# Kernel tuning notes

Hardware: AMD Instinct MI355X
Metric: run time of the kernel (lower is better)

The kernel has to match this reference:

```python
import jax, jax.numpy as jnp
import numpy as np

B, L, F, H, NC = 128, 1024, 128, 64, 16


def setup_inputs() -> dict:
    key = jax.random.key(0)
    ks = jax.random.split(key, 8)
    # strictly increasing timestamps -> each unique_consecutive group holds exactly
    # one event, so the torch group-mean over agg_c_t is a plain per-event update.
    t = jnp.broadcast_to(jnp.arange(L, dtype=jnp.float32), (B, L))
    m = jax.random.randint(ks[0], (B, L), 0, F).astype(jnp.float32)  # feature ids stored as float
    x = jax.random.normal(ks[1], (B, L), dtype=jnp.float32)
    delt = jax.random.uniform(ks[2], (B, L), dtype=jnp.float32)
    X = jnp.stack([t, m, x, delt], axis=1)  # [B, 4, L]
    lengths = jnp.full((B,), L, dtype=jnp.int32)
    s = 1.0 / np.sqrt(H + 1)
    W_gates = jax.random.uniform(ks[3], (F, 4 * H, H + 1), minval=-s, maxval=s)  # per-feature Linear(H+1 -> 4H)
    b_gates = jax.random.uniform(ks[4], (F, 4 * H), minval=-s, maxval=s)
    w_decay = jax.random.uniform(ks[5], (F,), minval=-1.0, maxval=1.0)  # per-feature Linear(1 -> 1)
    b_decay = jax.random.uniform(ks[6], (F,), minval=-1.0, maxval=1.0)
    in_dim = F * H + H  # concat(c_t, h_t.flatten()) -- default output branch
    so = 1.0 / np.sqrt(in_dim)
    W_out = jax.random.uniform(ks[7], (NC, in_dim), minval=-so, maxval=so)
    b_out = jnp.zeros((NC,), dtype=jnp.float32)
    return dict(X=X, lengths=lengths, W_gates=W_gates, b_gates=b_gates,
                w_decay=w_decay, b_decay=b_decay, W_out=W_out, b_out=b_out)


def _run_sample(x, delt, m, length, W_gates, b_gates, w_decay, b_decay):
    """Event-wise recurrence for one sample; returns concat(c_t, h_t.flatten())."""
    L_ = x.shape[0]
    F_, _, Hp1 = W_gates.shape
    H_ = Hp1 - 1

    def step(carry, ev):
        h_t, c_t = carry                     # h_t: [F,H], c_t: [H]
        mj, xj, dj, valid = ev
        # gated per-feature decay: exp(-max(0, w*dt + b)) (sr == 1)
        decay = jnp.exp(-jnp.maximum(0.0, w_decay[mj] * dj + b_decay[mj]))
        h_dec = decay * h_t[mj]
        inp = jnp.concatenate([xj[None], h_dec])            # [H+1]
        gates = W_gates[mj] @ inp + b_gates[mj]             # [4H]
        gi, gf, go, gc = jnp.split(gates, 4)
        c_new = jax.nn.sigmoid(gf) * c_t + jax.nn.sigmoid(gi) * jnp.tanh(gc)
        h_row = jax.nn.sigmoid(go) * jnp.tanh(c_new)
        c_t = jnp.where(valid, c_new, c_t)
        h_t = h_t.at[mj].set(jnp.where(valid, h_row, h_t[mj]))
        return (h_t, c_t), None

    valid = jnp.arange(L_) < length
    init = (jnp.zeros((F_, H_), x.dtype), jnp.zeros((H_,), x.dtype))
    (h_t, c_t), _ = jax.lax.scan(step, init, (m, x, delt, valid))
    return jnp.concatenate([c_t, h_t.reshape(-1)])          # [F*H + H]


def reference(X, lengths, W_gates, b_gates, w_decay, b_decay, W_out, b_out):
    m = X[:, 1].astype(jnp.int32)
    x = X[:, 2]
    delt = X[:, 3]
    feat = jax.vmap(lambda xi, di, mi, li: _run_sample(
        xi, di, mi, li, W_gates, b_gates, w_decay, b_decay))(x, delt, m, lengths)
    logits = feat @ W_out.T + b_out                          # [B, n_class]
    return jax.nn.softmax(logits, axis=-1)                   # torch softmax(dim=0) on 1-D vec per sample
```

## Files before the change

### kernel.cpp

```cpp
#include <hip/hip_runtime.h>
#include <cstdint>
#include <cstddef>

#define Bn 128
#define Ln 1024
#define Fn 128
#define Hn 64
#define NGn 256
#define NCn 16
#define IN_DIM (Hn + Fn*Hn)
#define NT 512
#define NREF 7

typedef float    f32x4 __attribute__((ext_vector_type(4)));
typedef float    f32x2 __attribute__((ext_vector_type(2)));
typedef _Float16 f16x8 __attribute__((ext_vector_type(8)));
typedef _Float16 f16x2 __attribute__((ext_vector_type(2)));

union U8 { f16x8 v; f16x2 p[4]; };

#define OFF_G    0
#define OFF_H    131072
#define OFF_PK   147456
#define OFF_MF   155648
#define OFF_PV   156672
#define OFF_NX   158720
#define OFF_RDY  160768
#define OFF_DON  161792
#define OFF_C    162816
#define OFF_RED  163072
#define OFF_LOG  163584
#define LDS_TOTAL 163648

__device__ __forceinline__ float fsigm(float x) {
    return __fdividef(1.0f, 1.0f + __expf(-x));
}
__device__ __forceinline__ float ftanh(float x) {
    float e = __expf(2.0f * x);
    return 1.0f - __fdividef(2.0f, e + 1.0f);
}
__device__ __forceinline__ float sigm_slow(float x) { return 1.0f / (1.0f + expf(-x)); }

#if __has_builtin(__builtin_amdgcn_fdot2)
#define DOT2(WP, HP, ACC) __builtin_amdgcn_fdot2((WP), (HP), (ACC), false)
#else
#define DOT2(WP, HP, ACC) fmaf((float)(WP)[0], (float)(HP)[0], \
                               fmaf((float)(WP)[1], (float)(HP)[1], (ACC)))
#endif

__global__ __launch_bounds__(256)
void prep_f16(const float* __restrict__ Wg, const float* __restrict__ bg,
              f16x8* __restrict__ Gw, f32x2* __restrict__ Gwb)
{
    const int m = blockIdx.x, r = threadIdx.x;
    const float* src = Wg + ((size_t)m * NGn + r) * 65;
    f32x2 wb; wb[0] = src[0]; wb[1] = bg[m * NGn + r];
    Gwb[((size_t)m << 8) + r] = wb;
#pragma unroll
    for (int c = 0; c < 8; ++c) {
        f16x8 v;
#pragma unroll
        for (int e = 0; e < 8; ++e) v[e] = (_Float16)src[1 + 8 * c + e];
        Gw[((size_t)m << 11) + (c << 8) + r] = v;
    }
}

__global__ __launch_bounds__(NT, 1)
void lstm_pre(const float* __restrict__ X, const int* __restrict__ lengths,
              const f16x8* __restrict__ Gw, const f32x2* __restrict__ Gwb,
              const float* __restrict__ wdec, const float* __restrict__ bdec,
              const float* __restrict__ Wo, const float* __restrict__ bo,
              float* __restrict__ out)
{
    extern __shared__ char smem[];
    float*    G_s  = (float*)(smem + OFF_G);
    _Float16* h16  = (_Float16*)(smem + OFF_H);
    f32x2*    pk_s = (f32x2*)(smem + OFF_PK);
    unsigned char* mf_s = (unsigned char*)(smem + OFF_MF);
    short*         pv_s = (short*)(smem + OFF_PV);
    short*         nx_s = (short*)(smem + OFF_NX);
    unsigned char* rdy  = (unsigned char*)(smem + OFF_RDY);
    unsigned char* don  = (unsigned char*)(smem + OFF_DON);
    float* c_s = (float*)(smem + OFF_C);
    int*   fo_s = (int*)(smem + OFF_RED);
    float* red_lds   = (float*)(smem + OFF_RED);
    float* logit_lds = (float*)(smem + OFF_LOG);

    const int b   = blockIdx.x;
    const int tid = threadIdx.x;
    const int l   = tid & 63;
    const int w   = tid >> 6;

    const float* mrow = X + ((size_t)b * 4 + 1) * Ln;
    const float* xrow = X + ((size_t)b * 4 + 2) * Ln;
    const float* drow = X + ((size_t)b * 4 + 3) * Ln;

    int len = lengths[b];
    if (len > Ln) len = Ln;

    if (tid < Fn) { G_s[tid] = wdec[tid]; G_s[Fn + tid] = bdec[tid]; }
    if (tid < Fn) fo_s[tid] = Ln;
    __syncthreads();
    for (int jj = tid; jj < Ln; jj += NT) {
        const int   m   = (int)mrow[jj];
        const float dec = __expf(-fmaxf(0.0f, fmaf(G_s[m], drow[jj], G_s[Fn + m])));
        f32x2 t; t[0] = xrow[jj]; t[1] = dec;
        pk_s[jj] = t;
        mf_s[jj] = (unsigned char)m;
        nx_s[jj] = -1;
        rdy[jj] = 0; don[jj] = 0;
    }
    __syncthreads();
    for (int j0 = tid; j0 < Ln; j0 += NT) {
        const int mm = (int)mf_s[j0];
        short pv = -1;
        for (int k = j0 - 1; k >= 0; --k)
            if ((int)mf_s[k] == mm) { pv = (short)k; break; }
        pv_s[j0] = pv;
        if (j0 < len) atomicMin(&fo_s[mm], j0);
    }
    __syncthreads();
    for (int j0 = tid; j0 < Ln; j0 += NT) {
        const int p = (int)pv_s[j0];
        if (p >= 0) nx_s[p] = (short)j0;
    }
    {
        f16x8 hzv;
#pragma unroll
        for (int e = 0; e < 8; ++e) hzv[e] = (_Float16)0.0f;
        for (int i = tid; i < (Fn * Hn / 8); i += NT) ((f16x8*)h16)[i] = hzv;
    }
    __syncthreads();
    for (int e = tid; e < Fn * NGn; e += NT) {
        const int m = e >> 8, r = e & 255;
        const int f0 = fo_s[m];
        if (f0 < len) {
            const float xv = pk_s[f0][0];
            const f32x2 wb = Gwb[((size_t)m << 8) + r];
            const int u = r & 63, g = r >> 6;
            G_s[(m << 8) + (u << 2) + g] = fmaf(xv, wb[0], wb[1]);
        }
    }
    __syncthreads();

    if (w == 0) {
        float cu = 0.0f;
        if (len > 0) {
            int m0 = (int)mf_s[0];
            int pv0 = (int)pv_s[0];
            int df0 = 1;
            asm volatile("" ::: "memory");
            f32x4 g0 = *(const f32x4*)(G_s + (m0 << 8) + (l << 2));
            for (int j = 0; j < len; ++j) {
                const int jn = (j + 1 < len) ? j + 1 : j;
                const int m1 = (int)mf_s[jn];
                const int pv1 = (int)pv_s[jn];
                const int pvc = (pv1 < 0) ? 0 : pv1;
                const int dfl = (int)*(volatile unsigned char*)(don + pvc);
                const int df1 = (pv1 < 0) ? 1 : dfl;
                asm volatile("" ::: "memory");
                f32x4 g1 = *(const f32x4*)(G_s + (m1 << 8) + (l << 2));
                if (!df0) {
                    while (*(volatile unsigned char*)(don + pv0) == 0)
                        asm volatile("s_sleep 1");
                    asm volatile("" ::: "memory");
                    g0 = *(const f32x4*)(G_s + (m0 << 8) + (l << 2));
                }
                const float cn = fmaf(fsigm(g0[1]), cu, fsigm(g0[0]) * ftanh(g0[3]));
                cu = cn;
                const float hv = fsigm(g0[2]) * ftanh(cn);
                h16[(m0 << 6) + l] = (_Float16)hv;
                asm volatile("s_waitcnt lgkmcnt(0)" ::: "memory");
                if (l == 0) *(volatile unsigned char*)(rdy + j) = 1;
                m0 = m1; pv0 = pv1; df0 = df1; g0 = g1;
            }
        }
        c_s[l] = cu;
    } else {
        for (int q = w - 1; q < len; q += NREF) {
            while (*(volatile unsigned char*)(rdy + q) == 0)
                asm volatile("s_sleep 1");
            asm volatile("" ::: "memory");
            const int m = (int)mf_s[q];
            const int jn = (int)nx_s[q];
            float xv = 0.0f, dc = 0.0f;
            f32x2 wb0, wb1, wb2, wb3;
            if (jn >= 0) {
                const f32x2 pkn = pk_s[jn];
                xv = pkn[0]; dc = pkn[1];
                const f32x2* bp = Gwb + ((size_t)m << 8) + l;
                wb0 = bp[0]; wb1 = bp[64]; wb2 = bp[128]; wb3 = bp[192];
            }
            U8 hr[8];
            {
                const f16x8* hp = (const f16x8*)(h16 + (m << 6));
#pragma unroll
                for (int c = 0; c < 8; ++c) hr[c].v = hp[c];
            }
            if (jn >= 0) {
                f32x4 accv;
#pragma unroll
                for (int g = 0; g < 4; ++g) {
                    const f16x8* wp = Gw + ((size_t)m << 11) + (g << 6) + l;
                    float acc = 0.0f;
#pragma unroll
                    for (int c = 0; c < 8; ++c) {
                        U8 wc; wc.v = wp[c << 8];
#pragma unroll
                        for (int e = 0; e < 4; ++e)
                            acc = DOT2(wc.p[e], hr[c].p[e], acc);
                    }
                    accv[g] = acc;
                }
                f32x4 gv;
                gv[0] = fmaf(dc, accv[0], fmaf(xv, wb0[0], wb0[1]));
                gv[1] = fmaf(dc, accv[1], fmaf(xv, wb1[0], wb1[1]));
                gv[2] = fmaf(dc, accv[2], fmaf(xv, wb2[0], wb2[1]));
                gv[3] = fmaf(dc, accv[3], fmaf(xv, wb3[0], wb3[1]));
                *(f32x4*)(G_s + (m << 8) + (l << 2)) = gv;
            }
            asm volatile("s_waitcnt lgkmcnt(0) vmcnt(0)" ::: "memory");
            if (l == 0) *(volatile unsigned char*)(don + q) = 1;
        }
    }
    __syncthreads();

    float p[NCn];
#pragma unroll
    for (int c = 0; c < NCn; ++c) p[c] = 0.0f;
    for (int i = tid; i < IN_DIM; i += NT) {
        const float fv = (i < Hn) ? c_s[i] : (float)h16[i - Hn];
#pragma unroll
        for (int c = 0; c < NCn; ++c)
            p[c] = fmaf(Wo[(size_t)c * IN_DIM + i], fv, p[c]);
    }
#pragma unroll
    for (int c = 0; c < NCn; ++c) {
        float v = p[c];
#pragma unroll
        for (int off = 32; off > 0; off >>= 1) v += __shfl_down(v, off, 64);
        if (l == 0) red_lds[w * NCn + c] = v;
    }
    __syncthreads();
    if (tid < NCn) {
        float s = bo[tid];
#pragma unroll
        for (int sw = 0; sw < (NT / 64); ++sw) s += red_lds[sw * NCn + tid];
        logit_lds[tid] = s;
    }
    __syncthreads();
    if (tid == 0) {
        float mx = logit_lds[0];
        for (int c = 1; c < NCn; ++c) mx = fmaxf(mx, logit_lds[c]);
        float e[NCn], sm = 0.0f;
        for (int c = 0; c < NCn; ++c) { e[c] = expf(logit_lds[c] - mx); sm += e[c]; }
        const float inv = 1.0f / sm;
        for (int c = 0; c < NCn; ++c) out[(size_t)b * NCn + c] = e[c] * inv;
    }
}

__global__ __launch_bounds__(256)
void lstm_fallback(const float* __restrict__ X, const int* __restrict__ lengths,
                   const float* __restrict__ Wg, const float* __restrict__ bg,
                   const float* __restrict__ wdec, const float* __restrict__ bdec,
                   const float* __restrict__ Wo, const float* __restrict__ bo,
                   float* __restrict__ out)
{
    __shared__ __align__(16) float h_lds[Fn * Hn];
    __shared__ float c_lds[Hn];
    __shared__ int   m_lds[Ln];
    __shared__ float x_lds[Ln];
    __shared__ float d_lds[Ln];
    __shared__ float wd_lds[Fn], bd_lds[Fn];
    __shared__ float red_lds[4 * NCn];
    __shared__ float logit_lds[NCn];

    const int b   = blockIdx.x;
    const int tid = threadIdx.x;
    const int l   = tid & 63;
    const int w   = tid >> 6;
    const int q   = l & 3;
    const int u   = w * 16 + (l >> 2);

    const float* mrow = X + ((size_t)b * 4 + 1) * Ln;
    const float* xrow = X + ((size_t)b * 4 + 2) * Ln;
    const float* drow = X + ((size_t)b * 4 + 3) * Ln;

    for (int i = tid; i < Fn * Hn; i += 256) h_lds[i] = 0.0f;
    if (tid < Hn) c_lds[tid] = 0.0f;
    if (tid < Fn) { wd_lds[tid] = wdec[tid]; bd_lds[tid] = bdec[tid]; }
    for (int i = tid; i < Ln; i += 256) {
        m_lds[i] = (int)mrow[i];
        x_lds[i] = xrow[i];
        d_lds[i] = drow[i];
    }
    __syncthreads();

    int len = lengths[b];
    if (len > Ln) len = Ln;
    const int g_raw = q * 64 + u;

    for (int j = 0; j < len; ++j) {
        const int   mj = m_lds[j];
        const float xj = x_lds[j];
        const float dj = d_lds[j];
        const float dec = expf(-fmaxf(0.0f, fmaf(wd_lds[mj], dj, bd_lds[mj])));
        const float4* hp = (const float4*)(h_lds + mj * Hn);
        const float* row = Wg + ((size_t)mj * NGn + g_raw) * 65;
        float acc = fmaf(row[0], xj, bg[mj * NGn + g_raw]);
        float a0 = 0.f, a1 = 0.f, a2 = 0.f, a3 = 0.f;
#pragma unroll
        for (int k4 = 0; k4 < 16; ++k4) {
            float4 hv = hp[k4];
            a0 = fmaf(row[1 + 4*k4 + 0], hv.x, a0);
            a1 = fmaf(row[1 + 4*k4 + 1], hv.y, a1);
            a2 = fmaf(row[1 + 4*k4 + 2], hv.z, a2);
            a3 = fmaf(row[1 + 4*k4 + 3], hv.w, a3);
        }
        acc = fmaf(dec, (a0 + a1) + (a2 + a3), acc);
        const int base = l & ~3;
        const float gi = __shfl(acc, base + 0, 64);
        const float gf = __shfl(acc, base + 1, 64);
        const float go = __shfl(acc, base + 2, 64);
        const float gc = __shfl(acc, base + 3, 64);
        __syncthreads();
        const float c_new = fmaf(sigm_slow(gf), c_lds[u], sigm_slow(gi) * tanhf(gc));
        if (q == 0) {
            c_lds[u] = c_new;
            h_lds[mj * Hn + u] = sigm_slow(go) * tanhf(c_new);
        }
        __syncthreads();
    }

    float p[NCn];
#pragma unroll
    for (int c = 0; c < NCn; ++c) p[c] = 0.0f;
    for (int i = tid; i < IN_DIM; i += 256) {
        const float fv = (i < Hn) ? c_lds[i] : h_lds[i - Hn];
#pragma unroll
        for (int c = 0; c < NCn; ++c)
            p[c] = fmaf(Wo[(size_t)c * IN_DIM + i], fv, p[c]);
    }
#pragma unroll
    for (int c = 0; c < NCn; ++c) {
        float v = p[c];
#pragma unroll
        for (int off = 32; off > 0; off >>= 1) v += __shfl_down(v, off, 64);
        if (l == 0) red_lds[w * NCn + c] = v;
    }
    __syncthreads();
    if (tid < NCn) {
        logit_lds[tid] = red_lds[tid] + red_lds[NCn + tid] +
                         red_lds[2 * NCn + tid] + red_lds[3 * NCn + tid] + bo[tid];
    }
    __syncthreads();
    if (tid == 0) {
        float mx = logit_lds[0];
        for (int c = 1; c < NCn; ++c) mx = fmaxf(mx, logit_lds[c]);
        float e[NCn], s = 0.0f;
        for (int c = 0; c < NCn; ++c) { e[c] = expf(logit_lds[c] - mx); s += e[c]; }
        const float inv = 1.0f / s;
        for (int c = 0; c < NCn; ++c) out[(size_t)b * NCn + c] = e[c] * inv;
    }
}

extern "C" void kernel_launch(void* const* d_in, const int* in_sizes, int n_in,
                              void* d_out, int out_size, void* d_ws, size_t ws_size,
                              hipStream_t stream)
{
    const float* X      = (const float*)d_in[0];
    const int*   len    = (const int*)  d_in[1];
    const float* Wg     = (const float*)d_in[2];
    const float* bg     = (const float*)d_in[3];
    const float* wdec   = (const float*)d_in[4];
    const float* bdec   = (const float*)d_in[5];
    const float* Wo     = (const float*)d_in[6];
    const float* bo     = (const float*)d_in[7];
    float*       out    = (float*)d_out;

    const size_t gw_bytes  = (size_t)Fn * 2048 * sizeof(f16x8);
    const size_t gwb_bytes = (size_t)Fn * 256 * sizeof(f32x2);
    const size_t need      = gw_bytes + gwb_bytes;

    if (ws_size >= need) {
        f16x8* Gw  = (f16x8*)d_ws;
        f32x2* Gwb = (f32x2*)((char*)d_ws + gw_bytes);
        prep_f16<<<Fn, 256, 0, stream>>>(Wg, bg, Gw, Gwb);
        (void)hipFuncSetAttribute((const void*)lstm_pre,
                                  hipFuncAttributeMaxDynamicSharedMemorySize,
                                  LDS_TOTAL);
        lstm_pre<<<Bn, NT, LDS_TOTAL, stream>>>(X, len, Gw, Gwb,
                                                wdec, bdec, Wo, bo, out);
    } else {
        lstm_fallback<<<Bn, 256, 0, stream>>>(X, len, Wg, bg,
                                              wdec, bdec, Wo, bo, out);
    }
}
```

Before: 568.2 us.

## Deepen recurrence prefetch and hoist weight loads ahead of the readiness spin-wait

The serial wave now keeps a three-step lookahead of feature ids, done flags and gate rows instead of one step. It also drops the explicit LDS wait before raising the ready flag and relies on in-order LDS completion. Helper waves load their 32 fp16 weight vectors and bias pairs before spinning on the ready flag, and they compute the four gate dot products with interleaved accumulators for more ILP. The aim is to take global-load latency and dependency stalls off the sequential critical path. The cost is much higher register pressure, and the removed waitcnts rely on memory-ordering assumptions.

```diff
diff --git a/kernel.cpp b/kernel.cpp
--- a/kernel.cpp
+++ b/kernel.cpp
@@ -146,20 +146,26 @@
     if (w == 0) {
         float cu = 0.0f;
         if (len > 0) {
-            int m0 = (int)mf_s[0];
-            int pv0 = (int)pv_s[0];
+            const int i1 = (1 < len) ? 1 : len - 1;
+            const int i2 = (2 < len) ? 2 : len - 1;
+            int m0 = (int)mf_s[0],  m1 = (int)mf_s[i1], m2 = (int)mf_s[i2];
+            int pv0 = (int)pv_s[0], pv1 = (int)pv_s[i1], pv2 = (int)pv_s[i2];
             int df0 = 1;
+            int df1 = (pv1 < 0) ? 1 : (int)*(volatile unsigned char*)(don + ((pv1 < 0) ? 0 : pv1));
+            int df2 = (pv2 < 0) ? 1 : (int)*(volatile unsigned char*)(don + ((pv2 < 0) ? 0 : pv2));
             asm volatile("" ::: "memory");
             f32x4 g0 = *(const f32x4*)(G_s + (m0 << 8) + (l << 2));
+            f32x4 g1 = *(const f32x4*)(G_s + (m1 << 8) + (l << 2));
+            f32x4 g2 = *(const f32x4*)(G_s + (m2 << 8) + (l << 2));
             for (int j = 0; j < len; ++j) {
-                const int jn = (j + 1 < len) ? j + 1 : j;
-                const int m1 = (int)mf_s[jn];
-                const int pv1 = (int)pv_s[jn];
-                const int pvc = (pv1 < 0) ? 0 : pv1;
-                const int dfl = (int)*(volatile unsigned char*)(don + pvc);
-                const int df1 = (pv1 < 0) ? 1 : dfl;
+                const int j3 = (j + 3 < len) ? j + 3 : len - 1;
+                const int m3 = (int)mf_s[j3];
+                const int pv3 = (int)pv_s[j3];
+                const int pvc = (pv3 < 0) ? 0 : pv3;
+                const int dq  = (int)*(volatile unsigned char*)(don + pvc);
+                const int df3 = (pv3 < 0) ? 1 : dq;
                 asm volatile("" ::: "memory");
-                f32x4 g1 = *(const f32x4*)(G_s + (m1 << 8) + (l << 2));
+                f32x4 g3 = *(const f32x4*)(G_s + (m3 << 8) + (l << 2));
                 if (!df0) {
                     while (*(volatile unsigned char*)(don + pv0) == 0)
                         asm volatile("s_sleep 1");
@@ -170,56 +176,63 @@
                 cu = cn;
                 const float hv = fsigm(g0[2]) * ftanh(cn);
                 h16[(m0 << 6) + l] = (_Float16)hv;
-                asm volatile("s_waitcnt lgkmcnt(0)" ::: "memory");
+                asm volatile("" ::: "memory");
                 if (l == 0) *(volatile unsigned char*)(rdy + j) = 1;
                 m0 = m1; pv0 = pv1; df0 = df1; g0 = g1;
+                m1 = m2; pv1 = pv2; df1 = df2; g1 = g2;
+                m2 = m3; pv2 = pv3; df2 = df3; g2 = g3;
             }
         }
         c_s[l] = cu;
     } else {
         for (int q = w - 1; q < len; q += NREF) {
-            while (*(volatile unsigned char*)(rdy + q) == 0)
-                asm volatile("s_sleep 1");
-            asm volatile("" ::: "memory");
-            const int m = (int)mf_s[q];
+            const int m  = (int)mf_s[q];
             const int jn = (int)nx_s[q];
-            float xv = 0.0f, dc = 0.0f;
-            f32x2 wb0, wb1, wb2, wb3;
             if (jn >= 0) {
-                const f32x2 pkn = pk_s[jn];
-                xv = pkn[0]; dc = pkn[1];
-                const f32x2* bp = Gwb + ((size_t)m << 8) + l;
-                wb0 = bp[0]; wb1 = bp[64]; wb2 = bp[128]; wb3 = bp[192];
-            }
-            U8 hr[8];
-            {
-                const f16x8* hp = (const f16x8*)(h16 + (m << 6));
-#pragma unroll
-                for (int c = 0; c < 8; ++c) hr[c].v = hp[c];
-            }
-            if (jn >= 0) {
-                f32x4 accv;
+                f16x8 wreg[32];
 #pragma unroll
                 for (int g = 0; g < 4; ++g) {
                     const f16x8* wp = Gw + ((size_t)m << 11) + (g << 6) + l;
-                    float acc = 0.0f;
-#pragma unroll
-                    for (int c = 0; c < 8; ++c) {
-                        U8 wc; wc.v = wp[c << 8];
-#pragma unroll
-                        for (int e = 0; e < 4; ++e)
-                            acc = DOT2(wc.p[e], hr[c].p[e], acc);
-                    }
-                    accv[g] = acc;
+#pragma unroll
+                    for (int c = 0; c < 8; ++c) wreg[g * 8 + c] = wp[c << 8];
+                }
+                const f32x2 pkn = pk_s[jn];
+                const float xv = pkn[0], dc = pkn[1];
+                const f32x2* bp = Gwb + ((size_t)m << 8) + l;
+                const f32x2 wb0 = bp[0], wb1 = bp[64], wb2 = bp[128], wb3 = bp[192];
+                while (*(volatile unsigned char*)(rdy + q) == 0)
+                    asm volatile("s_sleep 1");
+                asm volatile("" ::: "memory");
+                U8 hr[8];
+                {
+                    const f16x8* hp = (const f16x8*)(h16 + (m << 6));
+#pragma unroll
+                    for (int c = 0; c < 8; ++c) hr[c].v = hp[c];
                 }
                 f32x4 gv;
-                gv[0] = fmaf(dc, accv[0], fmaf(xv, wb0[0], wb0[1]));
-                gv[1] = fmaf(dc, accv[1], fmaf(xv, wb1[0], wb1[1]));
-                gv[2] = fmaf(dc, accv[2], fmaf(xv, wb2[0], wb2[1]));
-                gv[3] = fmaf(dc, accv[3], fmaf(xv, wb3[0], wb3[1]));
+                {
+                    float a0 = 0.f, a1 = 0.f, a2 = 0.f, a3 = 0.f;
+#pragma unroll
+                    for (int c = 0; c < 8; ++c) {
+                        U8 w0, w1, w2, w3;
+                        w0.v = wreg[c]; w1.v = wreg[8 + c];
+                        w2.v = wreg[16 + c]; w3.v = wreg[24 + c];
+#pragma unroll
+                        for (int e = 0; e < 4; ++e) {
+                            a0 = DOT2(w0.p[e], hr[c].p[e], a0);
+                            a1 = DOT2(w1.p[e], hr[c].p[e], a1);
+                            a2 = DOT2(w2.p[e], hr[c].p[e], a2);
+                            a3 = DOT2(w3.p[e], hr[c].p[e], a3);
+                        }
+                    }
+                    gv[0] = fmaf(dc, a0, fmaf(xv, wb0[0], wb0[1]));
+                    gv[1] = fmaf(dc, a1, fmaf(xv, wb1[0], wb1[1]));
+                    gv[2] = fmaf(dc, a2, fmaf(xv, wb2[0], wb2[1]));
+                    gv[3] = fmaf(dc, a3, fmaf(xv, wb3[0], wb3[1]));
+                }
                 *(f32x4*)(G_s + (m << 8) + (l << 2)) = gv;
+                asm volatile("" ::: "memory");
             }
-            asm volatile("s_waitcnt lgkmcnt(0) vmcnt(0)" ::: "memory");
             if (l == 0) *(volatile unsigned char*)(don + q) = 1;
         }
     }
```

After: 573.9 us. No clear change (+1.0%).
